# Optimization experiments

Measured on AMD Instinct MI355X. Metric: run time of the kernel, lower is better.

The kernel has to match this reference:

```python
import jax, jax.numpy as jnp
import numpy as np

MAX_SCALE = 10  # matches init_kwargs max_scale


def setup_inputs() -> dict:
    key = jax.random.key(0)
    # [B, H, W, D, C] as consumed by keras MaxPooling3D (channels_last)
    x = jax.random.normal(key, (8, 224, 224, 8, 8), dtype=jnp.float32)
    return {"x": x}


def reference(x):
    # For each scale s in 1..MAX_SCALE: max-pool over (H, W) with an s x s
    # window, stride 1, VALID padding (pool dim 3 has window 1), then sum the
    # pooled map over the two pooled spatial axes -> [B, D, C].
    boxes_at_scale = []
    for scale in range(1, MAX_SCALE + 1):
        pooled = jax.lax.reduce_window(
            x,
            -jnp.inf,
            jax.lax.max,
            window_dimensions=(1, scale, scale, 1, 1),
            window_strides=(1, 1, 1, 1, 1),
            padding="VALID",
        )  # [B, H-s+1, W-s+1, D, C]
        boxes_at_scale.append(jnp.sum(pooled, axis=(1, 2)))  # [B, D, C]
    stacked = jnp.stack(boxes_at_scale, axis=-1)  # [B, D, C, MAX_SCALE]
    return jax.nn.relu(stacked) + 1.0
```

## Files before the change

kernel.cpp:

```cpp
#include <hip/hip_runtime.h>

#define BB 8
#define HH 224
#define WW 224
#define DCH 64
#define NS 10
#define SEG_OUT 55
#define NSEG 5
#define STRIP 56
#define NSTRIP 4

__global__ void zero_kernel(float* out, int n) {
    int i = blockIdx.x * blockDim.x + threadIdx.x;
    if (i < n) out[i] = 0.0f;
}

__global__ void finalize_kernel(float* out, int n) {
    int i = blockIdx.x * blockDim.x + threadIdx.x;
    if (i < n) out[i] = fmaxf(out[i], 0.0f) + 1.0f;
}

__global__ __launch_bounds__(256, 2) void pool_kernel(const float* __restrict__ x,
                                                      float* __restrict__ out) {
    const int bid   = blockIdx.x;
    const int cgblk = bid & 3;
    const int ws    = (bid >> 2) % NSEG;
    const int hs    = ((bid >> 2) / NSEG) % NSTRIP;
    const int b     = bid / (4 * NSEG * NSTRIP);

    const int wave = threadIdx.x >> 6;
    const int lane = threadIdx.x & 63;
    const int ch   = cgblk * 16 + wave * 4;
    const int col  = ws * SEG_OUT + lane;
    const int row0 = hs * STRIP;
    const int rend = min(row0 + STRIP + (NS - 1), HH);

    float m[NS];
#pragma unroll
    for (int s = 1; s <= NS; ++s)
        m[s - 1] = (lane < SEG_OUT && col <= WW - s) ? 1.0f : 0.0f;

    float prev[NS - 1][4];
    float acc[NS][4];
#pragma unroll
    for (int s = 0; s < NS - 1; ++s)
#pragma unroll
        for (int c = 0; c < 4; ++c) prev[s][c] = 0.0f;
#pragma unroll
    for (int s = 0; s < NS; ++s)
#pragma unroll
        for (int c = 0; c < 4; ++c) acc[s][c] = 0.0f;

    const bool colok = (col < WW);
    const float* px = x + (((size_t)(b * HH + row0) * WW + col) * DCH + ch);
    const size_t rstride = (size_t)WW * DCH;

    float4 nxt = colok ? *(const float4*)px : make_float4(0.f, 0.f, 0.f, 0.f);

    for (int h = row0; h < rend; ++h) {
        float cp[4] = {nxt.x, nxt.y, nxt.z, nxt.w};
        if (h + 1 < rend) {
            px += rstride;
            if (colok) nxt = *(const float4*)px;
        }
        if (h < row0 + STRIP) {
#pragma unroll
            for (int c = 0; c < 4; ++c) acc[0][c] = fmaf(cp[c], m[0], acc[0][c]);
        }
#pragma unroll
        for (int s = 2; s <= NS; ++s) {
            float vmax[4], vn[4];
#pragma unroll
            for (int c = 0; c < 4; ++c) vmax[c] = fmaxf(prev[s - 2][c], cp[c]);
#pragma unroll
            for (int c = 0; c < 4; ++c) vn[c] = __shfl_down(vmax[c], 1);
#pragma unroll
            for (int c = 0; c < 4; ++c) prev[s - 2][c] = cp[c];
#pragma unroll
            for (int c = 0; c < 4; ++c) cp[c] = fmaxf(vmax[c], vn[c]);
            const int r = h - s + 1;
            if (r >= row0 && r < row0 + STRIP) {
#pragma unroll
                for (int c = 0; c < 4; ++c) acc[s - 1][c] = fmaf(cp[c], m[s - 1], acc[s - 1][c]);
            }
        }
    }

#pragma unroll
    for (int s = 0; s < NS; ++s) {
#pragma unroll
        for (int c = 0; c < 4; ++c) {
            float v = acc[s][c];
#pragma unroll
            for (int off = 32; off > 0; off >>= 1) v += __shfl_xor(v, off);
            if (lane == 0) atomicAdd(&out[((size_t)b * DCH + ch + c) * NS + s], v);
        }
    }
}

extern "C" void kernel_launch(void* const* d_in, const int* in_sizes, int n_in,
                              void* d_out, int out_size, void* d_ws, size_t ws_size,
                              hipStream_t stream) {
    const float* x = (const float*)d_in[0];
    float* out = (float*)d_out;
    const int nblk = (out_size + 255) / 256;
    zero_kernel<<<nblk, 256, 0, stream>>>(out, out_size);
    pool_kernel<<<BB * 4 * NSEG * NSTRIP, 256, 0, stream>>>(x, out);
    finalize_kernel<<<nblk, 256, 0, stream>>>(out, out_size);
}
```

Measured before the change: 224.2 us.

## Map lanes to channels and keep horizontal windows in registers per thread

Each lane now handles one of the 64 channels and walks a run of 8 output columns plus a 9-column halo, held in registers. The max-pyramid is built with in-register neighbour maxima instead of cross-lane shuffles, and an interior specialisation drops the boundary masks. Per-lane partial sums go straight to atomics without wave reductions, and the blocks are remapped across an 8-way interleave. The cost is a much larger register footprint (the pv and cp arrays), redundant halo loads, and more atomics on the output.

```diff
diff --git a/kernel.cpp b/kernel.cpp
--- a/kernel.cpp
+++ b/kernel.cpp
@@ -5,10 +5,12 @@
 #define WW 224
 #define DCH 64
 #define NS 10
-#define SEG_OUT 55
-#define NSEG 5
-#define STRIP 56
-#define NSTRIP 4
+#define GW 8
+#define SPAN (GW + NS - 1)
+#define STRIPR 14
+#define NSTRIPR 16
+#define NCB 7
+#define NBLK (BB * NSTRIPR * NCB)
 
 __global__ void zero_kernel(float* out, int n) {
     int i = blockIdx.x * blockDim.x + threadIdx.x;
@@ -20,82 +22,106 @@
     if (i < n) out[i] = fmaxf(out[i], 0.0f) + 1.0f;
 }
 
-__global__ __launch_bounds__(256, 2) void pool_kernel(const float* __restrict__ x,
-                                                      float* __restrict__ out) {
-    const int bid   = blockIdx.x;
-    const int cgblk = bid & 3;
-    const int ws    = (bid >> 2) % NSEG;
-    const int hs    = ((bid >> 2) / NSEG) % NSTRIP;
-    const int b     = bid / (4 * NSEG * NSTRIP);
+template<bool INTERIOR>
+__device__ __forceinline__ float maskedSum(const float* p, int w0, int s) {
+    if (INTERIOR) {
+        return ((p[0] + p[1]) + (p[2] + p[3])) + ((p[4] + p[5]) + (p[6] + p[7]));
+    } else {
+        float t = 0.0f;
+#pragma unroll
+        for (int k = 0; k < GW; ++k) t += (w0 + k <= WW - s) ? p[k] : 0.0f;
+        return t;
+    }
+}
 
-    const int wave = threadIdx.x >> 6;
-    const int lane = threadIdx.x & 63;
-    const int ch   = cgblk * 16 + wave * 4;
-    const int col  = ws * SEG_OUT + lane;
-    const int row0 = hs * STRIP;
-    const int rend = min(row0 + STRIP + (NS - 1), HH);
+template<bool INTERIOR>
+__device__ __forceinline__ void pool_body(const float* __restrict__ x,
+                                          float* __restrict__ out,
+                                          int b, int w0, int row0, int lane) {
+    const int rend = min(row0 + STRIPR + NS - 1, HH);
 
-    float m[NS];
+    float acc[NS];
 #pragma unroll
-    for (int s = 1; s <= NS; ++s)
-        m[s - 1] = (lane < SEG_OUT && col <= WW - s) ? 1.0f : 0.0f;
+    for (int s = 0; s < NS; ++s) acc[s] = 0.0f;
 
-    float prev[NS - 1][4];
-    float acc[NS][4];
+    float pv[NS - 1][SPAN];
 #pragma unroll
-    for (int s = 0; s < NS - 1; ++s)
+    for (int lv = 0; lv < NS - 1; ++lv)
 #pragma unroll
-        for (int c = 0; c < 4; ++c) prev[s][c] = 0.0f;
+        for (int w = 0; w < SPAN - lv; ++w) pv[lv][w] = 0.0f;
+
+    int koff[SPAN];
 #pragma unroll
-    for (int s = 0; s < NS; ++s)
+    for (int k = 0; k < SPAN; ++k) {
+        int c = INTERIOR ? (w0 + k) : min(w0 + k, WW - 1);
+        koff[k] = (c - w0 - 8) * DCH;
+    }
+
+    const float* px = x + (((size_t)(b * HH + row0) * WW + w0 + 8) * DCH + lane);
+    const ptrdiff_t rstride = (ptrdiff_t)WW * DCH;
+
+    float cp[SPAN];
 #pragma unroll
-        for (int c = 0; c < 4; ++c) acc[s][c] = 0.0f;
-
-    const bool colok = (col < WW);
-    const float* px = x + (((size_t)(b * HH + row0) * WW + col) * DCH + ch);
-    const size_t rstride = (size_t)WW * DCH;
-
-    float4 nxt = colok ? *(const float4*)px : make_float4(0.f, 0.f, 0.f, 0.f);
+    for (int k = 0; k < SPAN; ++k) cp[k] = px[koff[k]];
+    px += rstride;
 
     for (int h = row0; h < rend; ++h) {
-        float cp[4] = {nxt.x, nxt.y, nxt.z, nxt.w};
+        if (h < row0 + STRIPR) acc[0] += maskedSum<INTERIOR>(cp, w0, 1);
+
+        float vm[SPAN];
+#pragma unroll
+        for (int w = 0; w < SPAN; ++w) vm[w] = fmaxf(pv[0][w], cp[w]);
+#pragma unroll
+        for (int w = 0; w < SPAN; ++w) pv[0][w] = cp[w];
+
         if (h + 1 < rend) {
+#pragma unroll
+            for (int k = 0; k < SPAN; ++k) cp[k] = px[koff[k]];
             px += rstride;
-            if (colok) nxt = *(const float4*)px;
         }
-        if (h < row0 + STRIP) {
+
+        float c[SPAN - 1];
 #pragma unroll
-            for (int c = 0; c < 4; ++c) acc[0][c] = fmaf(cp[c], m[0], acc[0][c]);
-        }
+        for (int w = 0; w < SPAN - 1; ++w) c[w] = fmaxf(vm[w], vm[w + 1]);
+        if (h - 1 >= row0 && h - 1 < row0 + STRIPR)
+            acc[1] += maskedSum<INTERIOR>(c, w0, 2);
+
 #pragma unroll
-        for (int s = 2; s <= NS; ++s) {
-            float vmax[4], vn[4];
+        for (int lv = 1; lv < NS - 1; ++lv) {
+            const int wid = SPAN - lv;
+            float vm2[SPAN];
 #pragma unroll
-            for (int c = 0; c < 4; ++c) vmax[c] = fmaxf(prev[s - 2][c], cp[c]);
+            for (int w = 0; w < wid; ++w) vm2[w] = fmaxf(pv[lv][w], c[w]);
 #pragma unroll
-            for (int c = 0; c < 4; ++c) vn[c] = __shfl_down(vmax[c], 1);
+            for (int w = 0; w < wid; ++w) pv[lv][w] = c[w];
 #pragma unroll
-            for (int c = 0; c < 4; ++c) prev[s - 2][c] = cp[c];
-#pragma unroll
-            for (int c = 0; c < 4; ++c) cp[c] = fmaxf(vmax[c], vn[c]);
-            const int r = h - s + 1;
-            if (r >= row0 && r < row0 + STRIP) {
-#pragma unroll
-                for (int c = 0; c < 4; ++c) acc[s - 1][c] = fmaf(cp[c], m[s - 1], acc[s - 1][c]);
-            }
+            for (int w = 0; w < wid - 1; ++w) c[w] = fmaxf(vm2[w], vm2[w + 1]);
+            const int r = h - lv - 1;
+            if (r >= row0 && r < row0 + STRIPR)
+                acc[lv + 1] += maskedSum<INTERIOR>(c, w0, lv + 2);
         }
     }
 
+    float* ob = out + (size_t)(b * DCH + lane) * NS;
 #pragma unroll
-    for (int s = 0; s < NS; ++s) {
-#pragma unroll
-        for (int c = 0; c < 4; ++c) {
-            float v = acc[s][c];
-#pragma unroll
-            for (int off = 32; off > 0; off >>= 1) v += __shfl_xor(v, off);
-            if (lane == 0) atomicAdd(&out[((size_t)b * DCH + ch + c) * NS + s], v);
-        }
-    }
+    for (int s = 0; s < NS; ++s) atomicAdd(&ob[s], acc[s]);
+}
+
+__global__ __launch_bounds__(256, 2) void pool_kernel(const float* __restrict__ x,
+                                                      float* __restrict__ out) {
+    const int phys = blockIdx.x;
+    const int logical = (phys & 7) * (NBLK / 8) + (phys >> 3);
+    const int cb = logical % NCB;
+    const int hs = (logical / NCB) % NSTRIPR;
+    const int b  = logical / (NCB * NSTRIPR);
+
+    const int wv   = threadIdx.x >> 6;
+    const int lane = threadIdx.x & 63;
+    const int w0   = cb * (4 * GW) + wv * GW;
+    const int row0 = hs * STRIPR;
+
+    if (w0 + SPAN <= WW) pool_body<true>(x, out, b, w0, row0, lane);
+    else                 pool_body<false>(x, out, b, w0, row0, lane);
 }
 
 extern "C" void kernel_launch(void* const* d_in, const int* in_sizes, int n_in,
@@ -105,6 +131,6 @@
     float* out = (float*)d_out;
     const int nblk = (out_size + 255) / 256;
     zero_kernel<<<nblk, 256, 0, stream>>>(out, out_size);
-    pool_kernel<<<BB * 4 * NSEG * NSTRIP, 256, 0, stream>>>(x, out);
+    pool_kernel<<<NBLK, 256, 0, stream>>>(x, out);
     finalize_kernel<<<nblk, 256, 0, stream>>>(out, out_size);
 }
```

Result: slower. 275.0 us (+22.7%).

## Use DPP row shift, 2 channels per thread, phase-split row loop, block swizzle

Applied to the files above, without the earlier changes.

Each thread now handles 2 channels instead of 4, which halves register state so occupancy can rise (launch bounds go from 2 to 4 blocks per CU) and the block count doubles. The ds_bpermute-based __shfl_down is replaced by a DPP row-shift-left-by-1. The row loop is split into warm-up, steady and drain phases so the steady phase carries no per-level bounds checks. Block IDs are also swizzled across 8 groups. The DPP shift works within 16-lane rows and fills the row boundary with 0 (bound_ctrl), unlike the full-wavefront shift it replaces, which risks correctness at lanes 15, 31 and 47; float2 loads are also narrower than the previous float4 loads.

```diff
diff --git a/kernel.cpp b/kernel.cpp
--- a/kernel.cpp
+++ b/kernel.cpp
@@ -5,10 +5,12 @@
 #define WW 224
 #define DCH 64
 #define NS 10
-#define SEG_OUT 55
+#define SEG 55
 #define NSEG 5
 #define STRIP 56
-#define NSTRIP 4
+#define NHS 4
+#define NCG 8
+#define NBLK (BB * NCG * NSEG * NHS)
 
 __global__ void zero_kernel(float* out, int n) {
     int i = blockIdx.x * blockDim.x + threadIdx.x;
@@ -20,76 +22,94 @@
     if (i < n) out[i] = fmaxf(out[i], 0.0f) + 1.0f;
 }
 
-__global__ __launch_bounds__(256, 2) void pool_kernel(const float* __restrict__ x,
+__device__ __forceinline__ float dpp_shl1(float v) {
+    return __int_as_float(__builtin_amdgcn_update_dpp(
+        0, __float_as_int(v), 0x130, 0xF, 0xF, true));
+}
+
+template<int PHASE>
+__device__ __forceinline__ void row_body(int h, int row0, const float (&m)[NS],
+                                         float (&cp)[2], float (&prev)[NS - 1][2],
+                                         float (&acc)[NS][2]) {
+    if (PHASE != 2) {
+        acc[0][0] = fmaf(cp[0], m[0], acc[0][0]);
+        acc[0][1] = fmaf(cp[1], m[0], acc[0][1]);
+    }
+#pragma unroll
+    for (int lv = 0; lv < NS - 1; ++lv) {
+        float vm0 = fmaxf(prev[lv][0], cp[0]);
+        float vm1 = fmaxf(prev[lv][1], cp[1]);
+        prev[lv][0] = cp[0];
+        prev[lv][1] = cp[1];
+        cp[0] = fmaxf(vm0, dpp_shl1(vm0));
+        cp[1] = fmaxf(vm1, dpp_shl1(vm1));
+        bool on = true;
+        if (PHASE == 0) on = (h - lv - 1) >= row0;
+        if (PHASE == 2) on = (h - lv - 1) < row0 + STRIP;
+        if (on) {
+            acc[lv + 1][0] = fmaf(cp[0], m[lv + 1], acc[lv + 1][0]);
+            acc[lv + 1][1] = fmaf(cp[1], m[lv + 1], acc[lv + 1][1]);
+        }
+    }
+}
+
+__global__ __launch_bounds__(256, 4) void pool_kernel(const float* __restrict__ x,
                                                       float* __restrict__ out) {
-    const int bid   = blockIdx.x;
-    const int cgblk = bid & 3;
-    const int ws    = (bid >> 2) % NSEG;
-    const int hs    = ((bid >> 2) / NSEG) % NSTRIP;
-    const int b     = bid / (4 * NSEG * NSTRIP);
+    const int phys = blockIdx.x;
+    const int logical = (phys & 7) * (NBLK / 8) + (phys >> 3);
+    const int b = logical / (NCG * NSEG * NHS);
+    const int r = logical % (NCG * NSEG * NHS);
+    const int cg = r & 7;
+    const int ws = (r >> 3) % NSEG;
+    const int hs = (r >> 3) / NSEG;
 
-    const int wave = threadIdx.x >> 6;
+    const int wv   = threadIdx.x >> 6;
     const int lane = threadIdx.x & 63;
-    const int ch   = cgblk * 16 + wave * 4;
-    const int col  = ws * SEG_OUT + lane;
+    const int ch   = cg * 8 + wv * 2;
+    const int col  = ws * SEG + lane;
     const int row0 = hs * STRIP;
-    const int rend = min(row0 + STRIP + (NS - 1), HH);
+    const int rend = min(row0 + STRIP + NS - 1, HH);
 
     float m[NS];
 #pragma unroll
     for (int s = 1; s <= NS; ++s)
-        m[s - 1] = (lane < SEG_OUT && col <= WW - s) ? 1.0f : 0.0f;
+        m[s - 1] = (lane < SEG && col <= WW - s) ? 1.0f : 0.0f;
 
-    float prev[NS - 1][4];
-    float acc[NS][4];
+    float prev[NS - 1][2], acc[NS][2], cp[2], nv[2];
 #pragma unroll
-    for (int s = 0; s < NS - 1; ++s)
+    for (int lv = 0; lv < NS - 1; ++lv) { prev[lv][0] = 0.0f; prev[lv][1] = 0.0f; }
 #pragma unroll
-        for (int c = 0; c < 4; ++c) prev[s][c] = 0.0f;
-#pragma unroll
-    for (int s = 0; s < NS; ++s)
-#pragma unroll
-        for (int c = 0; c < 4; ++c) acc[s][c] = 0.0f;
+    for (int s = 0; s < NS; ++s) { acc[s][0] = 0.0f; acc[s][1] = 0.0f; }
+    nv[0] = 0.0f; nv[1] = 0.0f;
 
     const bool colok = (col < WW);
     const float* px = x + (((size_t)(b * HH + row0) * WW + col) * DCH + ch);
-    const size_t rstride = (size_t)WW * DCH;
+    const ptrdiff_t rstride = (ptrdiff_t)WW * DCH;
 
-    float4 nxt = colok ? *(const float4*)px : make_float4(0.f, 0.f, 0.f, 0.f);
+    if (colok) { float2 t = *(const float2*)px; nv[0] = t.x; nv[1] = t.y; }
 
-    for (int h = row0; h < rend; ++h) {
-        float cp[4] = {nxt.x, nxt.y, nxt.z, nxt.w};
-        if (h + 1 < rend) {
-            px += rstride;
-            if (colok) nxt = *(const float4*)px;
-        }
-        if (h < row0 + STRIP) {
-#pragma unroll
-            for (int c = 0; c < 4; ++c) acc[0][c] = fmaf(cp[c], m[0], acc[0][c]);
-        }
-#pragma unroll
-        for (int s = 2; s <= NS; ++s) {
-            float vmax[4], vn[4];
-#pragma unroll
-            for (int c = 0; c < 4; ++c) vmax[c] = fmaxf(prev[s - 2][c], cp[c]);
-#pragma unroll
-            for (int c = 0; c < 4; ++c) vn[c] = __shfl_down(vmax[c], 1);
-#pragma unroll
-            for (int c = 0; c < 4; ++c) prev[s - 2][c] = cp[c];
-#pragma unroll
-            for (int c = 0; c < 4; ++c) cp[c] = fmaxf(vmax[c], vn[c]);
-            const int r = h - s + 1;
-            if (r >= row0 && r < row0 + STRIP) {
-#pragma unroll
-                for (int c = 0; c < 4; ++c) acc[s - 1][c] = fmaf(cp[c], m[s - 1], acc[s - 1][c]);
-            }
-        }
+#define ROW_STEP(P)                                                          \
+    {                                                                        \
+        cp[0] = nv[0]; cp[1] = nv[1];                                        \
+        if (h + 1 < rend) {   \
+            px += rstride;                                                   \
+            if (colok) { float2 t = *(const float2*)px; nv[0] = t.x; nv[1] = t.y; } \
+        }                                                                    \
+        row_body<P>(h, row0, m, cp, prev, acc);                              \
     }
+
+    int h = row0;
+    const int warm_end = row0 + NS - 1;
+    for (; h < warm_end; ++h) ROW_STEP(0)
+    const int steady_end = min(row0 + STRIP, rend);
+    for (; h < steady_end; ++h) ROW_STEP(1)
+    for (; h < rend; ++h) ROW_STEP(2)
+#undef ROW_STEP
 
 #pragma unroll
     for (int s = 0; s < NS; ++s) {
 #pragma unroll
-        for (int c = 0; c < 4; ++c) {
+        for (int c = 0; c < 2; ++c) {
             float v = acc[s][c];
 #pragma unroll
             for (int off = 32; off > 0; off >>= 1) v += __shfl_xor(v, off);
@@ -105,6 +125,6 @@
     float* out = (float*)d_out;
     const int nblk = (out_size + 255) / 256;
     zero_kernel<<<nblk, 256, 0, stream>>>(out, out_size);
-    pool_kernel<<<BB * 4 * NSEG * NSTRIP, 256, 0, stream>>>(x, out);
+    pool_kernel<<<NBLK, 256, 0, stream>>>(x, out);
     finalize_kernel<<<nblk, 256, 0, stream>>>(out, out_size);
 }
```

Result: faster. 204.7 us (-8.7%).
